# Kernel optimization log

Measured on AMD Instinct MI355X. Metric: run time of the kernel, lower is better.

Reference implementation:

```python
import jax, jax.numpy as jnp
import numpy as np

N_NODES = 38000   # 19 feature types x ~2000 categories
IN_DIM = 64
HID = 128         # hid_num in source
R = 8             # number of relations
E = 200000        # edges per relation
N_ROWS = 60000    # data rows
F = 19            # len(features)
N_CLASSES = 10


def setup_inputs() -> dict:
    key = jax.random.key(0)
    ks = jax.random.split(key, 20)
    s_in = 1.0 / np.sqrt(IN_DIM)
    s_h = 1.0 / np.sqrt(HID)
    inp = {
        "node_feats": jax.random.normal(ks[0], (N_NODES, IN_DIM), jnp.float32),
        "edges_src": jax.random.randint(ks[1], (R, E), 0, N_NODES),
        "edges_dst": jax.random.randint(ks[2], (R, E), 0, N_NODES),
        "row_idx": jax.random.randint(ks[3], (N_ROWS, F), 0, N_NODES),
        "row_mask": jax.random.randint(ks[4], (N_ROWS, F), 0, 2).astype(bool),
        # input linear
        "W_in": jax.random.normal(ks[5], (IN_DIM, HID), jnp.float32) * s_in,
        "b_in": jnp.zeros((HID,), jnp.float32),
        # RGCN layer 1 and 2: per-relation GraphConv weights
        "W1": jax.random.normal(ks[6], (R, HID, HID), jnp.float32) * s_h,
        "b1": jnp.zeros((R, HID), jnp.float32),
        "W2": jax.random.normal(ks[7], (R, HID, HID), jnp.float32) * s_h,
        "b2": jnp.zeros((R, HID), jnp.float32),
        # MLP head
        "Wm1": jax.random.normal(ks[8], (HID, HID), jnp.float32) * s_h,
        "bm1": jnp.zeros((HID,), jnp.float32),
        "Wm2": jax.random.normal(ks[9], (HID, HID), jnp.float32) * s_h,
        "bm2": jnp.zeros((HID,), jnp.float32),
        "Wm3": jax.random.normal(ks[10], (HID, N_CLASSES), jnp.float32) * s_h,
        "bm3": jnp.zeros((N_CLASSES,), jnp.float32),
    }
    return inp


def _hetero_conv(h, src, dst, W, b):
    """DGL HeteroGraphConv(sum) of GraphConv(norm='both') over R relations."""
    n = h.shape[0]
    out = jnp.zeros((n, W.shape[2]), h.dtype)
    ones = jnp.ones((src.shape[1],), h.dtype)
    for r in range(src.shape[0]):
        deg_out = jax.ops.segment_sum(ones, src[r], num_segments=n)
        deg_in = jax.ops.segment_sum(ones, dst[r], num_segments=n)
        norm_s = jnp.where(deg_out > 0, deg_out, 1.0) ** -0.5
        norm_d = jnp.where(deg_in > 0, deg_in, 1.0) ** -0.5
        msg = h[src[r]] * norm_s[src[r], None]            # [E, hid]
        agg = jax.ops.segment_sum(msg, dst[r], num_segments=n)
        out = out + (agg * norm_d[:, None]) @ W[r] + b[r]
    return out


def reference(node_feats, edges_src, edges_dst, row_idx, row_mask,
              W_in, b_in, W1, b1, W2, b2, Wm1, bm1, Wm2, bm2, Wm3, bm3):
    # input linear + relu (applied to every node type's features)
    h = jax.nn.relu(node_feats @ W_in + b_in)            # [N_nodes, HID]
    # 2-layer RGCN
    h = jax.nn.relu(_hetero_conv(h, edges_src, edges_dst, W1, b1))
    h = _hetero_conv(h, edges_src, edges_dst, W2, b2)    # [N_nodes, HID]
    # vectorized ragged gather + masked mean (replaces per-row python loop)
    m = row_mask.astype(h.dtype)                          # [N_rows, F]
    emb = h[row_idx] * m[..., None]                       # [N_rows, F, HID]
    cnt = jnp.maximum(m.sum(-1, keepdims=True), 1.0)
    mean_feat = emb.sum(1) / cnt                          # [N_rows, HID]
    # MLP head
    x = jax.nn.relu(mean_feat @ Wm1 + bm1)
    x = jax.nn.relu(x @ Wm2 + bm2)
    return x @ Wm3 + bm3                                  # [N_rows, N_CLASSES]
```

## Files before the change

### kernel.cpp

```cpp
#include <hip/hip_runtime.h>
#include <hip/hip_bf16.h>

#define NN    38000
#define HID   128
#define RR    8
#define EE    200000
#define NROWS 60000
#define FF    19
#define NCLS  10
#define NRD   (RR*NN)
#define HB    38912
#define CH    16
#define CE    (EE/CH)

typedef __hip_bfloat16 bf16;
typedef __attribute__((ext_vector_type(8))) short short8;
typedef __attribute__((ext_vector_type(4))) float floatx4;

__device__ __forceinline__ float b2f(bf16 x){ return __bfloat162float(x); }
__device__ __forceinline__ bf16  f2b(float x){ return __float2bfloat16(x); }

__device__ __forceinline__ int geti(const void* a, long long i, int wide){
  return wide ? (int)(((const long long*)a)[i]) : ((const int*)a)[i];
}

__global__ void k_fill(float* out, int n, float v){
  int i = blockIdx.x*256 + threadIdx.x;
  if (i < n) out[i] = v;
}

__global__ void k_sniff(const void* mask, const void* ridx, const void* esrc, int* flags){
  int lane = threadIdx.x;
  const unsigned short* mu = (const unsigned short*)mask;
  int l3f80e=0, l3f80o=0, lbytehi=0, loddnz=0, lother=0;
  for (int i = lane; i < 4096; i += 64){
    unsigned v = mu[i];
    if (v == 0) continue;
    if (v == 0x3F80){ if (i & 1) l3f80o = 1; else l3f80e = 1; continue; }
    unsigned lo = v & 0xFF, hi = v >> 8;
    int lob = (lo == 0 || lo == 1 || lo == 0xFF);
    int hib = (hi == 0 || hi == 1 || hi == 0xFF);
    if (lob && hib){ if (hi) lbytehi = 1; if (i & 1) loddnz = 1; continue; }
    lother = 1;
  }
  int a3f80e = __any(l3f80e);
  int a3f80o = __any(l3f80o);
  int abytehi = __any(lbytehi);
  int aoddnz = __any(loddnz);
  int aother = __any(lother);
  int mtype = -1;
  if (!aother){
    if (a3f80e && !abytehi && !aoddnz)       mtype = 2;
    else if (a3f80o && !a3f80e && !abytehi)  mtype = 3;
    else if (!a3f80e && !a3f80o){
      if (abytehi || aoddnz) mtype = 1;
      else                   mtype = 0;
    }
  }
  const int* es = (const int*)esrc;
  int loddE = 0, lseenE = 0;
  for (int i = lane; i < 512; i += 64){
    if (es[2*i+1] != 0) loddE = 1;
    if (es[2*i] > 1)    lseenE = 1;
  }
  int fE = (!__any(loddE) && __any(lseenE)) ? 1 : 0;
  const int* ri = (const int*)ridx;
  int loddI = 0, lseenI = 0;
  for (int i = lane; i < 512; i += 64){
    if (ri[2*i+1] != 0) loddI = 1;
    if (ri[2*i] > 1)    lseenI = 1;
  }
  int fI = (!__any(loddI) && __any(lseenI)) ? 1 : 0;
  if (lane == 0){ flags[1] = mtype; flags[3] = fE; flags[4] = fI; }
}


__global__ __launch_bounds__(1024) void kg_hist(const void* esrc, const void* edst,
                                                int* __restrict__ ghd, int* __restrict__ ghs,
                                                const int* flags){
  __shared__ int hist[HB];
  int t = threadIdx.x;
  for (int i = t; i < HB; i += 1024) hist[i] = 0;
  __syncthreads();
  int b = blockIdx.x;
  int side = b >> 7;
  int r = (b >> 4) & 7, c = b & 15;
  int wide = flags[3];
  const void* e = side ? esrc : edst;
  long long base = (long long)r*EE + (long long)c*CE;
  if (!wide){
    const int* p = (const int*)e + base;
    for (int i = t; i < CE; i += 1024) atomicAdd(&hist[p[i]], 1);
  } else {
    const long long* p = (const long long*)e + base;
    for (int i = t; i < CE; i += 1024) atomicAdd(&hist[(int)p[i]], 1);
  }
  __syncthreads();
  int* out = (side ? ghs : ghd) + (long long)(r*CH + c)*HB;
  for (int i = t; i < HB; i += 1024) out[i] = hist[i];
}

__global__ void kg_tot(const int* __restrict__ ghd, const int* __restrict__ ghs,
                       int* __restrict__ totg, float* __restrict__ ns){
  int i = blockIdx.x*256 + threadIdx.x;
  if (i >= RR*HB) return;
  int r = i / HB, bin = i - r*HB;
  int sd = 0, ss = 0;
#pragma unroll
  for (int c = 0; c < CH; c++){
    sd += ghd[(long long)(r*CH+c)*HB + bin];
    ss += ghs[(long long)(r*CH+c)*HB + bin];
  }
  totg[i] = sd;
  if (bin < NN) ns[r*NN + bin] = rsqrtf((float)(ss > 0 ? ss : 1));
}

__global__ __launch_bounds__(1024) void kg_scan(const int* __restrict__ totg,
                                                int* __restrict__ rowptr){
  __shared__ int tot[HB];
  __shared__ int wsum[16];
  int t = threadIdx.x, r = blockIdx.x;
  for (int i = t; i < HB; i += 1024) tot[i] = totg[r*HB + i];
  __syncthreads();
  int b0 = t*38;
  int loc[38], s = 0;
#pragma unroll
  for (int j = 0; j < 38; j++){ loc[j] = s; s += tot[b0+j]; }
  int lane = t & 63, w = t >> 6;
  int sc = s;
  for (int off = 1; off < 64; off <<= 1){
    int v = __shfl_up(sc, off);
    if (lane >= off) sc += v;
  }
  if (lane == 63) wsum[w] = sc;
  __syncthreads();
  if (t < 16){
    int v = wsum[t];
    int scw = v;
    for (int off = 1; off < 16; off <<= 1){
      int u = __shfl_up(scw, off);
      if (t >= off) scw += u;
    }
    wsum[t] = scw - v;
  }
  __syncthreads();
  int base = r*EE + (sc - s) + wsum[w];
#pragma unroll
  for (int j = 0; j < 38; j++) tot[b0+j] = base + loc[j];
  __syncthreads();
  for (int i = t; i < NN; i += 1024) rowptr[r*NN + i] = tot[i];
  if (r == RR-1 && t == 0) rowptr[NRD] = RR*EE;
}

__global__ void kg_curs(const int* __restrict__ ghd, const int* __restrict__ rowptr,
                        int* __restrict__ gcurs){
  int i = blockIdx.x*256 + threadIdx.x;
  if (i >= NRD) return;
  int r = i / NN, bin = i - r*NN;
  int p = rowptr[i];
#pragma unroll
  for (int c = 0; c < CH; c++){
    gcurs[(long long)(r*CH+c)*HB + bin] = p;
    p += ghd[(long long)(r*CH+c)*HB + bin];
  }
}

__global__ __launch_bounds__(1024) void kg_scatter(const void* esrc, const void* edst,
                                                   const int* __restrict__ gcurs,
                                                   const float* __restrict__ ns,
                                                   int2* __restrict__ csrw, const int* flags){
  __shared__ int cur[HB];
  int t = threadIdx.x, b = blockIdx.x;
  int r = b >> 4, c = b & 15;
  const int* g = gcurs + (long long)(r*CH + c)*HB;
  for (int i = t; i < HB; i += 1024) cur[i] = g[i];
  __syncthreads();
  if (b == 0 && t < 8){ int2 z; z.x = 0; z.y = 0; csrw[RR*EE + t] = z; }
  int wide = flags[3];
  const float* nsr = ns + r*NN;
  long long base = (long long)r*EE + (long long)c*CE;
  if (!wide){
    const int* ps = (const int*)esrc + base;
    const int* pd = (const int*)edst + base;
    for (int i = t; i < CE; i += 1024){
      int d = pd[i], s = ps[i];
      int pos = atomicAdd(&cur[d], 1);
      int2 v; v.x = s; v.y = __float_as_int(nsr[s]);
      csrw[pos] = v;
    }
  } else {
    const long long* ps = (const long long*)esrc + base;
    const long long* pd = (const long long*)edst + base;
    for (int i = t; i < CE; i += 1024){
      int d = (int)pd[i], s = (int)ps[i];
      int pos = atomicAdd(&cur[d], 1);
      int2 v; v.x = s; v.y = __float_as_int(nsr[s]);
      csrw[pos] = v;
    }
  }
}


__global__ void k_bias(const float* b_in, const float* b1, const float* b2,
                       const float* bm1, const float* bm2, const float* bm3, float* o){
  int t = threadIdx.x;
  o[t] = b_in[t];
  float s1 = 0.f, s2 = 0.f;
  for (int r = 0; r < RR; r++){ s1 += b1[r*HID+t]; s2 += b2[r*HID+t]; }
  o[128+t] = s1; o[256+t] = s2;
  o[384+t] = bm1[t]; o[512+t] = bm2[t];
  if (t < NCLS) o[640+t] = bm3[t];
}

__global__ void k_packall(const float* __restrict__ W1, const float* __restrict__ W2,
                          const float* __restrict__ Wm1, const float* __restrict__ Wm2,
                          bf16* __restrict__ W1p, bf16* __restrict__ W2p,
                          bf16* __restrict__ Wm1p, bf16* __restrict__ Wm2p){
  int idx0 = blockIdx.x*256 + threadIdx.x;
  if (idx0 < 4*65536){
    const float* W = (idx0 < 2*65536) ? W1 : W2;
    bf16* out      = (idx0 < 2*65536) ? W1p : W2p;
    int idx = idx0 & (2*65536 - 1);
    int j = idx & 7;
    int l = (idx >> 3) & 63;
    int t = (idx >> 9) & 127;
    int g = idx >> 16;
    int ktg = t & 15, nt = t >> 4;
    int kglob = ktg*32 + ((l>>4)<<3) + j;
    int rel = kglob >> 7;
    int krow = kglob & 127;
    int n = nt*16 + (l&15);
    out[idx] = f2b(W[((g*4 + rel)*128 + krow)*128 + n]);
  } else if (idx0 < 4*65536 + 2*16384){
    int t2 = idx0 - 4*65536;
    const float* B = (t2 < 16384) ? Wm1 : Wm2;
    bf16* out      = (t2 < 16384) ? Wm1p : Wm2p;
    int idx = t2 & 16383;
    int j  = idx & 7;
    int l  = (idx >> 3) & 63;
    int t  = idx >> 9;
    int kt = t & 3;
    int nt = t >> 2;
    int k = kt*32 + ((l>>4)<<3) + j;
    int n = nt*16 + (l&15);
    out[idx] = f2b(B[k*128 + n]);
  }
}

__global__ void k_gemm_in(const float* __restrict__ A, const float* __restrict__ B,
                          const float* bias, bf16* __restrict__ out){
  int row0 = blockIdx.x * 4;
  int col = threadIdx.x;
  float a0=0.f, a1=0.f, a2=0.f, a3=0.f;
  for (int k = 0; k < 64; k++){
    float bv = B[k*HID + col];
    a0 += A[(long long)(row0+0)*64 + k] * bv;
    a1 += A[(long long)(row0+1)*64 + k] * bv;
    a2 += A[(long long)(row0+2)*64 + k] * bv;
    a3 += A[(long long)(row0+3)*64 + k] * bv;
  }
  float bb = bias[col];
  out[(long long)(row0+0)*HID + col] = f2b(fmaxf(a0 + bb, 0.f));
  out[(long long)(row0+1)*HID + col] = f2b(fmaxf(a1 + bb, 0.f));
  out[(long long)(row0+2)*HID + col] = f2b(fmaxf(a2 + bb, 0.f));
  out[(long long)(row0+3)*HID + col] = f2b(fmaxf(a3 + bb, 0.f));
}

#define LOADW(Q, base_) \
  Q##0 = cw[(base_)+0]; Q##1 = cw[(base_)+1]; Q##2 = cw[(base_)+2]; Q##3 = cw[(base_)+3]; \
  Q##4 = cw[(base_)+4]; Q##5 = cw[(base_)+5]; Q##6 = cw[(base_)+6]; Q##7 = cw[(base_)+7];

#define GATHW(P, Q) \
  P##0 = hv[(long long)(int)Q##0*64 + lane]; \
  P##1 = hv[(long long)(int)Q##1*64 + lane]; \
  P##2 = hv[(long long)(int)Q##2*64 + lane]; \
  P##3 = hv[(long long)(int)Q##3*64 + lane]; \
  P##4 = hv[(long long)(int)Q##4*64 + lane]; \
  P##5 = hv[(long long)(int)Q##5*64 + lane]; \
  P##6 = hv[(long long)(int)Q##6*64 + lane]; \
  P##7 = hv[(long long)(int)Q##7*64 + lane];

#define ACCE(Qv, Pv, cond) { \
  float wk_ = (cond) ? __int_as_float((int)((Qv) >> 32)) : 0.f; \
  acc0 += wk_ * __uint_as_float((Pv) << 16); \
  acc1 += wk_ * __uint_as_float((Pv) & 0xffff0000u); }

#define ROWBODY(i, QC, PC, QN, PN) { \
  int b_ = __builtin_amdgcn_readfirstlane(__shfl(rp, (i))); \
  int e_ = __builtin_amdgcn_readfirstlane(__shfl(rp, (i)+1)); \
  LOADW(QN, e_)                        \
  GATHW(PN, QN)                        \
  float acc0 = 0.f, acc1 = 0.f; \
  ACCE(QC##0, PC##0, b_+0 < e_) \
  ACCE(QC##1, PC##1, b_+1 < e_) \
  ACCE(QC##2, PC##2, b_+2 < e_) \
  ACCE(QC##3, PC##3, b_+3 < e_) \
  ACCE(QC##4, PC##4, b_+4 < e_) \
  ACCE(QC##5, PC##5, b_+5 < e_) \
  ACCE(QC##6, PC##6, b_+6 < e_) \
  ACCE(QC##7, PC##7, b_+7 < e_) \
  for (int j = b_ + 8; j < e_; j += 8){       \
    unsigned long long q0 = cw[j],   q1 = cw[j+1], q2 = cw[j+2], q3 = cw[j+3]; \
    unsigned long long q4 = cw[j+4], q5 = cw[j+5], q6 = cw[j+6], q7 = cw[j+7]; \
    unsigned p0 = hv[(long long)(int)q0*64 + lane]; \
    unsigned p1 = hv[(long long)(int)q1*64 + lane]; \
    unsigned p2 = hv[(long long)(int)q2*64 + lane]; \
    unsigned p3 = hv[(long long)(int)q3*64 + lane]; \
    unsigned p4 = hv[(long long)(int)q4*64 + lane]; \
    unsigned p5 = hv[(long long)(int)q5*64 + lane]; \
    unsigned p6 = hv[(long long)(int)q6*64 + lane]; \
    unsigned p7 = hv[(long long)(int)q7*64 + lane]; \
    ACCE(q0, p0, 1) \
    ACCE(q1, p1, j+1 < e_) \
    ACCE(q2, p2, j+2 < e_) \
    ACCE(q3, p3, j+3 < e_) \
    ACCE(q4, p4, j+4 < e_) \
    ACCE(q5, p5, j+5 < e_) \
    ACCE(q6, p6, j+6 < e_) \
    ACCE(q7, p7, j+7 < e_) \
  } \
  int deg = e_ - b_; \
  float nd = rsqrtf((float)(deg > 0 ? deg : 1)); \
  bf16 o0 = f2b(acc0 * nd), o1 = f2b(acc1 * nd); \
  unsigned ov = ((unsigned)(*(unsigned short*)&o1) << 16) | (*(unsigned short*)&o0); \
  int addr = (w << 12) + ((i) << 8) + (lane << 2); \
  addr ^= (((i) & 7) << 4); \
  *(unsigned*)(lds + addr) = ov; }

__global__ __launch_bounds__(512) void k_layer(const bf16* __restrict__ h,
                                               const int* __restrict__ rowptr,
                                               const unsigned long long* __restrict__ cw,
                                               const bf16* __restrict__ Bp,
                                               const float* __restrict__ bias,
                                               bf16* __restrict__ hout, int relu){
  __shared__ char lds[8*16*256];
  int w = threadIdx.x >> 6;
  int lane = threadIdx.x & 63;
  int d0 = blockIdx.x << 4;
  const unsigned* hv = (const unsigned*)h;

  int rp = 0;
  if (lane < 17) rp = rowptr[w*NN + d0 + lane];

  unsigned long long qa0,qa1,qa2,qa3,qa4,qa5,qa6,qa7;
  unsigned long long qb0,qb1,qb2,qb3,qb4,qb5,qb6,qb7;
  unsigned pa0,pa1,pa2,pa3,pa4,pa5,pa6,pa7;
  unsigned pb0,pb1,pb2,pb3,pb4,pb5,pb6,pb7;

  {
    int b0_ = __builtin_amdgcn_readfirstlane(__shfl(rp, 0));
    LOADW(qa, b0_)
    GATHW(pa, qa)
  }
  ROWBODY( 0, qa, pa, qb, pb)
  ROWBODY( 1, qb, pb, qa, pa)
  ROWBODY( 2, qa, pa, qb, pb)
  ROWBODY( 3, qb, pb, qa, pa)
  ROWBODY( 4, qa, pa, qb, pb)
  ROWBODY( 5, qb, pb, qa, pa)
  ROWBODY( 6, qa, pa, qb, pb)
  ROWBODY( 7, qb, pb, qa, pa)
  ROWBODY( 8, qa, pa, qb, pb)
  ROWBODY( 9, qb, pb, qa, pa)
  ROWBODY(10, qa, pa, qb, pb)
  ROWBODY(11, qb, pb, qa, pa)
  ROWBODY(12, qa, pa, qb, pb)
  ROWBODY(13, qb, pb, qa, pa)
  ROWBODY(14, qa, pa, qb, pb)
  ROWBODY(15, qb, pb, qa, pa)
  __syncthreads();

  floatx4 acc = (floatx4){0.f,0.f,0.f,0.f};
  int row = lane & 15;
  int kb = (lane >> 4) << 4;
#pragma unroll
  for (int rel = 0; rel < 8; rel++){
    int half = rel >> 2;
    const bf16* bp = Bp + half*65536 + lane*8 + (w*16 + (rel & 3)*4)*512;
#pragma unroll
    for (int ktl = 0; ktl < 4; ktl++){
      int off = (row << 8) + ktl*64 + kb;
      off ^= ((row & 7) << 4);
      short8 a = *(const short8*)(lds + (rel << 12) + off);
      short8 b = *(const short8*)(bp + ktl*512);
      acc = __builtin_amdgcn_mfma_f32_16x16x32_bf16(a, b, acc, 0, 0, 0);
    }
  }
  int col = w*16 + (lane & 15);
  int row0 = d0 + ((lane >> 4) << 2);
  float bb = bias[col];
#pragma unroll
  for (int v = 0; v < 4; v++){
    float x = acc[v] + bb;
    if (relu) x = fmaxf(x, 0.f);
    hout[(long long)(row0 + v)*HID + col] = f2b(x);
  }
}

__global__ void k_mfma_out(const bf16* __restrict__ A, const bf16* __restrict__ Bp,
                           const float* __restrict__ bias, bf16* __restrict__ out, int M){
  int wave = (blockIdx.x*blockDim.x + threadIdx.x) >> 6;
  int lane = threadIdx.x & 63;
  int rowBase = wave << 4;
  if (rowBase >= M) return;
  long long aRow = rowBase + (lane & 15);
  int kGrp = (lane >> 4) << 3;
  floatx4 acc[8];
#pragma unroll
  for (int nt = 0; nt < 8; nt++) acc[nt] = (floatx4){0.f,0.f,0.f,0.f};
  const bf16* bp = Bp + lane*8;
#pragma unroll
  for (int kt = 0; kt < 4; kt++){
    short8 a = *(const short8*)(A + aRow*HID + kt*32 + kGrp);
#pragma unroll
    for (int nt = 0; nt < 8; nt++){
      short8 b = *(const short8*)(bp + (nt*4 + kt)*512);
      acc[nt] = __builtin_amdgcn_mfma_f32_16x16x32_bf16(a, b, acc[nt], 0, 0, 0);
    }
  }
  int colB = lane & 15;
  int rowQ = rowBase + ((lane >> 4) << 2);
#pragma unroll
  for (int nt = 0; nt < 8; nt++){
    int col = nt*16 + colB;
    float bb = bias[col];
#pragma unroll
    for (int v = 0; v < 4; v++)
      out[(long long)(rowQ+v)*HID + col] = f2b(fmaxf(acc[nt][v] + bb, 0.f));
  }
}

__global__ void k_mean(const bf16* __restrict__ h, const void* ridx, const void* rmask,
                       const int* flags, bf16* __restrict__ mean){
  int row = blockIdx.x*4 + (threadIdx.x >> 6);
  int lane = threadIdx.x & 63;
  int mt = flags[1];
  int wide = flags[4];
  const int* m4            = (const int*)rmask;
  const unsigned char* m1  = (const unsigned char*)rmask;
  const unsigned short* m2 = (const unsigned short*)rmask;
  const unsigned int* mw   = (const unsigned int*)rmask;
  const unsigned* hv = (const unsigned*)h;
  int on = 0, idxl = 0;
  if (lane < FF){
    long long i = (long long)row*FF + lane;
    if      (mt == 1) on = (m1[i] != 0);
    else if (mt == 2) on = (m2[i] != 0);
    else if (mt == 3) on = (mw[i] != 0);
    else              on = (m4[i] != 0);
    if (on) idxl = geti(ridx, i, wide);
  }
  unsigned long long bal = __ballot(on);
  float cnt = (float)__popcll(bal);
  float acc0 = 0.f, acc1 = 0.f;
#pragma unroll
  for (int j = 0; j < FF; j++){
    int s = __shfl(idxl, j);
    float w = (float)((bal >> j) & 1ull);
    unsigned pv = hv[(long long)s*64 + lane];
    acc0 += w * __uint_as_float(pv << 16);
    acc1 += w * __uint_as_float(pv & 0xffff0000u);
  }
  float inv = 1.f / fmaxf(cnt, 1.f);
  bf16 o0 = f2b(acc0 * inv), o1 = f2b(acc1 * inv);
  unsigned ov = ((unsigned)(*(unsigned short*)&o1) << 16) | (*(unsigned short*)&o0);
  ((unsigned*)mean)[(long long)row*64 + lane] = ov;
}

__global__ void k_last(const bf16* __restrict__ A, const float* __restrict__ B,
                       const float* bias, float* __restrict__ out){
  int i = blockIdx.x*256 + threadIdx.x;
  if (i >= NROWS*NCLS) return;
  int row = i / NCLS, col = i - row*NCLS;
  float acc = bias[col];
  const bf16* ar = A + (long long)row*HID;
  for (int k = 0; k < HID; k++) acc += b2f(ar[k]) * B[k*NCLS + col];
  out[i] = acc;
}

extern "C" void kernel_launch(void* const* d_in, const int* in_sizes, int n_in,
                              void* d_out, int out_size, void* d_ws, size_t ws_size,
                              hipStream_t stream){
  float* out = (float*)d_out;

  static const int expect[17] = {
    NN*64, RR*EE, RR*EE, NROWS*FF, NROWS*FF,
    64*HID, HID, RR*HID*HID, RR*HID, RR*HID*HID, RR*HID,
    HID*HID, HID, HID*HID, HID, HID*NCLS, NCLS };
  bool ok = (n_in >= 17) && (out_size == NROWS*NCLS);
  if (ok) for (int i = 0; i < 17; i++) if (in_sizes[i] != expect[i]) { ok = false; break; }
  if (!ok){
    k_fill<<<(NROWS*NCLS+255)/256, 256, 0, stream>>>(out, NROWS*NCLS, 64.0f);
    return;
  }

  const void*  e_src = d_in[1];
  const void*  e_dst = d_in[2];
  const void*  ridx  = d_in[3];
  const void*  rmask = d_in[4];
  const float* nf   = (const float*)d_in[0];
  const float* W_in = (const float*)d_in[5];
  const float* b_in = (const float*)d_in[6];
  const float* W1   = (const float*)d_in[7];
  const float* b1   = (const float*)d_in[8];
  const float* W2   = (const float*)d_in[9];
  const float* b2   = (const float*)d_in[10];
  const float* Wm1  = (const float*)d_in[11];
  const float* bm1  = (const float*)d_in[12];
  const float* Wm2  = (const float*)d_in[13];
  const float* bm2  = (const float*)d_in[14];
  const float* Wm3  = (const float*)d_in[15];
  const float* bm3  = (const float*)d_in[16];

  char* ws = (char*)d_ws;
  size_t off = 0;
  auto take = [&](size_t bytes)->char*{
    char* p = ws + off; off += (bytes + 255) & ~(size_t)255; return p; };

  int*   flags  = (int*)  take(256);
  char*  rgn    =         take(58368000);
  bf16*  meanb  = (bf16*) (rgn);
  bf16*  x1     = (bf16*) (rgn + 15360000);
  bf16*  x2     = (bf16*) (rgn + 30720000);
  int*   ghd    = (int*)  (rgn);
  int*   ghs    = (int*)  (rgn + 19922944);
  int*   gcurs  = (int*)  (rgn + 19922944);
  int*   totg   = (int*)  (rgn + 39845888);
  bf16*  h1     = (bf16*) take((size_t)NN*HID*2);
  bf16*  h2     = (bf16*) take((size_t)NN*HID*2);
  int*   rowptr = (int*)  take((size_t)(NRD+1)*4);
  int2*  csrw   = (int2*) take((size_t)RR*EE*8 + 64);
  float* ns     = (float*)take((size_t)NRD*4);
  float* bias   = (float*)take(656*4);
  bf16*  W1p    = (bf16*) take((size_t)2*65536*2);
  bf16*  W2p    = (bf16*) take((size_t)2*65536*2);
  bf16*  Wm1p   = (bf16*) take((size_t)16384*2);
  bf16*  Wm2p   = (bf16*) take((size_t)16384*2);

  if (off > ws_size){
    k_fill<<<(NROWS*NCLS+255)/256, 256, 0, stream>>>(out, NROWS*NCLS, 32.0f);
    return;
  }

  k_sniff   <<<1, 64, 0, stream>>>(rmask, ridx, e_src, flags);
  kg_hist   <<<256, 1024, 0, stream>>>(e_src, e_dst, ghd, ghs, flags);
  kg_tot    <<<(RR*HB+255)/256, 256, 0, stream>>>(ghd, ghs, totg, ns);
  kg_scan   <<<RR, 1024, 0, stream>>>(totg, rowptr);
  kg_curs   <<<(NRD+255)/256, 256, 0, stream>>>(ghd, rowptr, gcurs);
  kg_scatter<<<128, 1024, 0, stream>>>(e_src, e_dst, gcurs, ns, csrw, flags);
  k_bias    <<<1, 128, 0, stream>>>(b_in, b1, b2, bm1, bm2, bm3, bias);

  k_packall<<<(4*65536 + 2*16384 + 255)/256, 256, 0, stream>>>(W1, W2, Wm1, Wm2,
                                                               W1p, W2p, Wm1p, Wm2p);

  k_gemm_in<<<NN/4, 128, 0, stream>>>(nf, W_in, bias+0, h1);

  k_layer<<<NN/16, 512, 0, stream>>>(h1, rowptr, (const unsigned long long*)csrw,
                                     W1p, bias+128, h2, 1);
  k_layer<<<NN/16, 512, 0, stream>>>(h2, rowptr, (const unsigned long long*)csrw,
                                     W2p, bias+256, h1, 0);

  k_mean<<<NROWS/4, 256, 0, stream>>>(h1, ridx, rmask, flags, meanb);

  int gR = (NROWS/16 + 3)/4;
  k_mfma_out<<<gR, 256, 0, stream>>>(meanb, Wm1p, bias+384, x1, NROWS);
  k_mfma_out<<<gR, 256, 0, stream>>>(x1,    Wm2p, bias+512, x2, NROWS);
  k_last<<<(NROWS*NCLS+255)/256, 256, 0, stream>>>(x2, Wm3, bias+640, out);
}
```

Before: 460.7 us.

## Fuse masked mean and MLP head into one kernel; shrink CSR-build histograms

Merges the masked-mean gather, both hidden MLP GEMMs and the final 10-class projection into a single kernel per 16 rows. Intermediates stay in swizzled LDS instead of round-tripping through global memory, which removes three launches and the HBM traffic for the mean, x1 and x2 buffers. Separately, the CSR build halves the edge chunks per relation (16 to 8) and stores per-chunk histograms as 16-bit counts, reducing histogram memory traffic at the cost of fewer blocks in the hist/scatter kernels. The last layer is computed by a small scalar loop reading LDS, which could become a minor bottleneck.

```diff
diff --git a/kernel.cpp b/kernel.cpp
--- a/kernel.cpp
+++ b/kernel.cpp
@@ -10,7 +10,7 @@
 #define NCLS  10
 #define NRD   (RR*NN)
 #define HB    38912
-#define CH    16
+#define CH    8
 #define CE    (EE/CH)
 
 typedef __hip_bfloat16 bf16;
@@ -76,15 +76,16 @@
 
 
 __global__ __launch_bounds__(1024) void kg_hist(const void* esrc, const void* edst,
-                                                int* __restrict__ ghd, int* __restrict__ ghs,
+                                                unsigned short* __restrict__ ghd,
+                                                unsigned short* __restrict__ ghs,
                                                 const int* flags){
   __shared__ int hist[HB];
   int t = threadIdx.x;
   for (int i = t; i < HB; i += 1024) hist[i] = 0;
   __syncthreads();
   int b = blockIdx.x;
-  int side = b >> 7;
-  int r = (b >> 4) & 7, c = b & 15;
+  int side = b >> 6;
+  int r = (b >> 3) & 7, c = b & 7;
   int wide = flags[3];
   const void* e = side ? esrc : edst;
   long long base = (long long)r*EE + (long long)c*CE;
@@ -96,11 +97,12 @@
     for (int i = t; i < CE; i += 1024) atomicAdd(&hist[(int)p[i]], 1);
   }
   __syncthreads();
-  int* out = (side ? ghs : ghd) + (long long)(r*CH + c)*HB;
-  for (int i = t; i < HB; i += 1024) out[i] = hist[i];
-}
-
-__global__ void kg_tot(const int* __restrict__ ghd, const int* __restrict__ ghs,
+  unsigned short* out = (side ? ghs : ghd) + (long long)(r*CH + c)*HB;
+  for (int i = t; i < HB; i += 1024) out[i] = (unsigned short)hist[i];
+}
+
+__global__ void kg_tot(const unsigned short* __restrict__ ghd,
+                       const unsigned short* __restrict__ ghs,
                        int* __restrict__ totg, float* __restrict__ ns){
   int i = blockIdx.x*256 + threadIdx.x;
   if (i >= RR*HB) return;
@@ -152,7 +154,8 @@
   if (r == RR-1 && t == 0) rowptr[NRD] = RR*EE;
 }
 
-__global__ void kg_curs(const int* __restrict__ ghd, const int* __restrict__ rowptr,
+__global__ void kg_curs(const unsigned short* __restrict__ ghd,
+                        const int* __restrict__ rowptr,
                         int* __restrict__ gcurs){
   int i = blockIdx.x*256 + threadIdx.x;
   if (i >= NRD) return;
@@ -171,7 +174,7 @@
                                                    int2* __restrict__ csrw, const int* flags){
   __shared__ int cur[HB];
   int t = threadIdx.x, b = blockIdx.x;
-  int r = b >> 4, c = b & 15;
+  int r = b >> 3, c = b & 7;
   const int* g = gcurs + (long long)(r*CH + c)*HB;
   for (int i = t; i < HB; i += 1024) cur[i] = g[i];
   __syncthreads();
@@ -397,43 +400,19 @@
   }
 }
 
-__global__ void k_mfma_out(const bf16* __restrict__ A, const bf16* __restrict__ Bp,
-                           const float* __restrict__ bias, bf16* __restrict__ out, int M){
-  int wave = (blockIdx.x*blockDim.x + threadIdx.x) >> 6;
+__global__ __launch_bounds__(256) void k_head(const bf16* __restrict__ h,
+                                              const void* ridx, const void* rmask,
+                                              const int* __restrict__ flags,
+                                              const bf16* __restrict__ Wm1p,
+                                              const bf16* __restrict__ Wm2p,
+                                              const float* __restrict__ Wm3,
+                                              const float* __restrict__ bias,
+                                              float* __restrict__ out){
+  __shared__ char ldsA[16*256];
+  __shared__ char ldsB[16*256];
+  int wv = threadIdx.x >> 6;
   int lane = threadIdx.x & 63;
-  int rowBase = wave << 4;
-  if (rowBase >= M) return;
-  long long aRow = rowBase + (lane & 15);
-  int kGrp = (lane >> 4) << 3;
-  floatx4 acc[8];
-#pragma unroll
-  for (int nt = 0; nt < 8; nt++) acc[nt] = (floatx4){0.f,0.f,0.f,0.f};
-  const bf16* bp = Bp + lane*8;
-#pragma unroll
-  for (int kt = 0; kt < 4; kt++){
-    short8 a = *(const short8*)(A + aRow*HID + kt*32 + kGrp);
-#pragma unroll
-    for (int nt = 0; nt < 8; nt++){
-      short8 b = *(const short8*)(bp + (nt*4 + kt)*512);
-      acc[nt] = __builtin_amdgcn_mfma_f32_16x16x32_bf16(a, b, acc[nt], 0, 0, 0);
-    }
-  }
-  int colB = lane & 15;
-  int rowQ = rowBase + ((lane >> 4) << 2);
-#pragma unroll
-  for (int nt = 0; nt < 8; nt++){
-    int col = nt*16 + colB;
-    float bb = bias[col];
-#pragma unroll
-    for (int v = 0; v < 4; v++)
-      out[(long long)(rowQ+v)*HID + col] = f2b(fmaxf(acc[nt][v] + bb, 0.f));
-  }
-}
-
-__global__ void k_mean(const bf16* __restrict__ h, const void* ridx, const void* rmask,
-                       const int* flags, bf16* __restrict__ mean){
-  int row = blockIdx.x*4 + (threadIdx.x >> 6);
-  int lane = threadIdx.x & 63;
+  int r0 = blockIdx.x << 4;
   int mt = flags[1];
   int wide = flags[4];
   const int* m4            = (const int*)rmask;
@@ -441,41 +420,117 @@
   const unsigned short* m2 = (const unsigned short*)rmask;
   const unsigned int* mw   = (const unsigned int*)rmask;
   const unsigned* hv = (const unsigned*)h;
-  int on = 0, idxl = 0;
-  if (lane < FF){
-    long long i = (long long)row*FF + lane;
-    if      (mt == 1) on = (m1[i] != 0);
-    else if (mt == 2) on = (m2[i] != 0);
-    else if (mt == 3) on = (mw[i] != 0);
-    else              on = (m4[i] != 0);
-    if (on) idxl = geti(ridx, i, wide);
-  }
-  unsigned long long bal = __ballot(on);
-  float cnt = (float)__popcll(bal);
-  float acc0 = 0.f, acc1 = 0.f;
-#pragma unroll
-  for (int j = 0; j < FF; j++){
-    int s = __shfl(idxl, j);
-    float w = (float)((bal >> j) & 1ull);
-    unsigned pv = hv[(long long)s*64 + lane];
-    acc0 += w * __uint_as_float(pv << 16);
-    acc1 += w * __uint_as_float(pv & 0xffff0000u);
-  }
-  float inv = 1.f / fmaxf(cnt, 1.f);
-  bf16 o0 = f2b(acc0 * inv), o1 = f2b(acc1 * inv);
-  unsigned ov = ((unsigned)(*(unsigned short*)&o1) << 16) | (*(unsigned short*)&o0);
-  ((unsigned*)mean)[(long long)row*64 + lane] = ov;
-}
-
-__global__ void k_last(const bf16* __restrict__ A, const float* __restrict__ B,
-                       const float* bias, float* __restrict__ out){
-  int i = blockIdx.x*256 + threadIdx.x;
-  if (i >= NROWS*NCLS) return;
-  int row = i / NCLS, col = i - row*NCLS;
-  float acc = bias[col];
-  const bf16* ar = A + (long long)row*HID;
-  for (int k = 0; k < HID; k++) acc += b2f(ar[k]) * B[k*NCLS + col];
-  out[i] = acc;
+
+  for (int rr = 0; rr < 4; rr++){
+    int tr = wv*4 + rr;
+    int row = r0 + tr;
+    int on = 0, idxl = 0;
+    if (lane < FF){
+      long long i = (long long)row*FF + lane;
+      if      (mt == 1) on = (m1[i] != 0);
+      else if (mt == 2) on = (m2[i] != 0);
+      else if (mt == 3) on = (mw[i] != 0);
+      else              on = (m4[i] != 0);
+      if (on) idxl = geti(ridx, i, wide);
+    }
+    unsigned long long bal = __ballot(on);
+    float cnt = (float)__popcll(bal);
+    float acc0 = 0.f, acc1 = 0.f;
+#pragma unroll
+    for (int j = 0; j < FF; j++){
+      int s = __shfl(idxl, j);
+      float wgt = (float)((bal >> j) & 1ull);
+      unsigned pv = hv[(long long)s*64 + lane];
+      acc0 += wgt * __uint_as_float(pv << 16);
+      acc1 += wgt * __uint_as_float(pv & 0xffff0000u);
+    }
+    float inv = 1.f / fmaxf(cnt, 1.f);
+    bf16 o0 = f2b(acc0 * inv), o1 = f2b(acc1 * inv);
+    unsigned ov = ((unsigned)(*(unsigned short*)&o1) << 16) | (*(unsigned short*)&o0);
+    int addr = (tr << 8) + (lane << 2);
+    addr ^= ((tr & 7) << 4);
+    *(unsigned*)(ldsA + addr) = ov;
+  }
+  __syncthreads();
+
+  int arow = lane & 15;
+  int kb = (lane >> 4) << 4;
+  int colB = lane & 15;
+  int rowQ = (lane >> 4) << 2;
+
+  {
+    floatx4 accA = (floatx4){0.f,0.f,0.f,0.f};
+    floatx4 accB = (floatx4){0.f,0.f,0.f,0.f};
+    const bf16* bp = Wm1p + lane*8;
+#pragma unroll
+    for (int kt = 0; kt < 4; kt++){
+      int off = (arow << 8) + kt*64 + kb;
+      off ^= ((arow & 7) << 4);
+      short8 a = *(const short8*)(ldsA + off);
+      short8 b0 = *(const short8*)(bp + ((wv*2+0)*4 + kt)*512);
+      short8 b1 = *(const short8*)(bp + ((wv*2+1)*4 + kt)*512);
+      accA = __builtin_amdgcn_mfma_f32_16x16x32_bf16(a, b0, accA, 0, 0, 0);
+      accB = __builtin_amdgcn_mfma_f32_16x16x32_bf16(a, b1, accB, 0, 0, 0);
+    }
+#pragma unroll
+    for (int ntl = 0; ntl < 2; ntl++){
+      int col = (wv*2 + ntl)*16 + colB;
+      float bb = bias[384 + col];
+#pragma unroll
+      for (int v = 0; v < 4; v++){
+        float x = ((ntl == 0) ? accA[v] : accB[v]) + bb;
+        bf16 xv = f2b(fmaxf(x, 0.f));
+        int rowi = rowQ + v;
+        int addr = (rowi << 8) + col*2;
+        addr ^= ((rowi & 7) << 4);
+        *(unsigned short*)(ldsB + addr) = *(unsigned short*)&xv;
+      }
+    }
+  }
+  __syncthreads();
+
+  {
+    floatx4 accA = (floatx4){0.f,0.f,0.f,0.f};
+    floatx4 accB = (floatx4){0.f,0.f,0.f,0.f};
+    const bf16* bp = Wm2p + lane*8;
+#pragma unroll
+    for (int kt = 0; kt < 4; kt++){
+      int off = (arow << 8) + kt*64 + kb;
+      off ^= ((arow & 7) << 4);
+      short8 a = *(const short8*)(ldsB + off);
+      short8 b0 = *(const short8*)(bp + ((wv*2+0)*4 + kt)*512);
+      short8 b1 = *(const short8*)(bp + ((wv*2+1)*4 + kt)*512);
+      accA = __builtin_amdgcn_mfma_f32_16x16x32_bf16(a, b0, accA, 0, 0, 0);
+      accB = __builtin_amdgcn_mfma_f32_16x16x32_bf16(a, b1, accB, 0, 0, 0);
+    }
+#pragma unroll
+    for (int ntl = 0; ntl < 2; ntl++){
+      int col = (wv*2 + ntl)*16 + colB;
+      float bb = bias[512 + col];
+#pragma unroll
+      for (int v = 0; v < 4; v++){
+        float x = ((ntl == 0) ? accA[v] : accB[v]) + bb;
+        bf16 xv = f2b(fmaxf(x, 0.f));
+        int rowi = rowQ + v;
+        int addr = (rowi << 8) + col*2;
+        addr ^= ((rowi & 7) << 4);
+        *(unsigned short*)(ldsA + addr) = *(unsigned short*)&xv;
+      }
+    }
+  }
+  __syncthreads();
+
+  for (int t = threadIdx.x; t < 16*NCLS; t += 256){
+    int tr = t / NCLS, col = t - tr*NCLS;
+    float acc = bias[640 + col];
+    for (int k = 0; k < HID; k++){
+      int addr = (tr << 8) + k*2;
+      addr ^= ((tr & 7) << 4);
+      unsigned short uv = *(const unsigned short*)(ldsA + addr);
+      acc += b2f(*(bf16*)&uv) * Wm3[k*NCLS + col];
+    }
+    out[(long long)(r0 + tr)*NCLS + col] = acc;
+  }
 }
 
 extern "C" void kernel_launch(void* const* d_in, const int* in_sizes, int n_in,
@@ -519,13 +574,10 @@
 
   int*   flags  = (int*)  take(256);
   char*  rgn    =         take(58368000);
-  bf16*  meanb  = (bf16*) (rgn);
-  bf16*  x1     = (bf16*) (rgn + 15360000);
-  bf16*  x2     = (bf16*) (rgn + 30720000);
-  int*   ghd    = (int*)  (rgn);
-  int*   ghs    = (int*)  (rgn + 19922944);
-  int*   gcurs  = (int*)  (rgn + 19922944);
-  int*   totg   = (int*)  (rgn + 39845888);
+  unsigned short* ghd = (unsigned short*)(rgn);
+  unsigned short* ghs = (unsigned short*)(rgn + 4980736);
+  int*   gcurs  = (int*)  (rgn +  9961472);
+  int*   totg   = (int*)  (rgn + 19922944);
   bf16*  h1     = (bf16*) take((size_t)NN*HID*2);
   bf16*  h2     = (bf16*) take((size_t)NN*HID*2);
   int*   rowptr = (int*)  take((size_t)(NRD+1)*4);
@@ -543,11 +595,11 @@
   }
 
   k_sniff   <<<1, 64, 0, stream>>>(rmask, ridx, e_src, flags);
-  kg_hist   <<<256, 1024, 0, stream>>>(e_src, e_dst, ghd, ghs, flags);
+  kg_hist   <<<128, 1024, 0, stream>>>(e_src, e_dst, ghd, ghs, flags);
   kg_tot    <<<(RR*HB+255)/256, 256, 0, stream>>>(ghd, ghs, totg, ns);
   kg_scan   <<<RR, 1024, 0, stream>>>(totg, rowptr);
   kg_curs   <<<(NRD+255)/256, 256, 0, stream>>>(ghd, rowptr, gcurs);
-  kg_scatter<<<128, 1024, 0, stream>>>(e_src, e_dst, gcurs, ns, csrw, flags);
+  kg_scatter<<<64, 1024, 0, stream>>>(e_src, e_dst, gcurs, ns, csrw, flags);
   k_bias    <<<1, 128, 0, stream>>>(b_in, b1, b2, bm1, bm2, bm3, bias);
 
   k_packall<<<(4*65536 + 2*16384 + 255)/256, 256, 0, stream>>>(W1, W2, Wm1, Wm2,
@@ -560,10 +612,5 @@
   k_layer<<<NN/16, 512, 0, stream>>>(h2, rowptr, (const unsigned long long*)csrw,
                                      W2p, bias+256, h1, 0);
 
-  k_mean<<<NROWS/4, 256, 0, stream>>>(h1, ridx, rmask, flags, meanb);
-
-  int gR = (NROWS/16 + 3)/4;
-  k_mfma_out<<<gR, 256, 0, stream>>>(meanb, Wm1p, bias+384, x1, NROWS);
-  k_mfma_out<<<gR, 256, 0, stream>>>(x1,    Wm2p, bias+512, x2, NROWS);
-  k_last<<<(NROWS*NCLS+255)/256, 256, 0, stream>>>(x2, Wm3, bias+640, out);
-}
+  k_head<<<NROWS/16, 256, 0, stream>>>(h1, ridx, rmask, flags, Wm1p, Wm2p, Wm3, bias, out);
+}
```

Measured after the change: 440.4 us. 1.05x faster.
